# Optimization experiments

Measured on AMD Instinct MI355X. Metric: run time of the kernel, lower is better.

## Reference

```python
import jax, jax.numpy as jnp
import numpy as np

INV_TEMP = 10.0

def pairwise_distance(x, y):
    # squared L2 distance: [b,n,c],[b,m,c] -> [b,n,m]
    x2 = jnp.sum(x * x, axis=-1, keepdims=True)          # [b,n,1]
    y2 = jnp.sum(y * y, axis=-1)[:, None, :]             # [b,1,m]
    xy = jnp.einsum('bnc,bmc->bnm', x, y)                # [b,n,m]
    return x2 + y2 - 2.0 * xy

def setup_inputs() -> dict:
    key = jax.random.key(0)
    k1, k2, k3 = jax.random.split(key, 3)
    b, n, m, c = 4, 4096, 4096, 32
    x_f = jax.random.normal(k1, (b, n, c), dtype=jnp.float32)
    y_f = jax.random.normal(k2, (b, m, c), dtype=jnp.float32)
    y_c = jax.random.normal(k3, (b, m, 3), dtype=jnp.float32)
    temp_inv = jnp.ones((1,), dtype=jnp.float32) * INV_TEMP
    return {"x_f": x_f, "y_f": y_f, "y_c": y_c, "temp_inv": temp_inv}

def reference(x_f, y_f, y_c, temp_inv):
    # corr_type='soft', st=True (straight-through)
    dist = pairwise_distance(x_f, y_f)                   # [b,n,m]
    y_soft = jax.nn.softmax(-dist * temp_inv[0], axis=2) # [b,n,m]
    index = jnp.argmax(y_soft, axis=2)                   # [b,n]
    y_hard = jax.nn.one_hot(index, y_soft.shape[2], dtype=y_soft.dtype)
    ret = y_hard - jax.lax.stop_gradient(y_soft) + y_soft
    x_corr = jnp.matmul(ret, y_c)                        # [b,n,3]
    return x_corr
```

## Files before the change

### kernel.cpp

```cpp
#include <hip/hip_runtime.h>

#define B 4
#define N 4096
#define M 4096
#define C 32
#define BN (B * N)
#define MS 16

typedef short bf16x8 __attribute__((ext_vector_type(8)));
typedef float f32x4  __attribute__((ext_vector_type(4)));
typedef unsigned int u32x4 __attribute__((ext_vector_type(4)));

#define WS_WI ((size_t)MS * BN * 4)
#define WS_YP (WS_WI * 2)
#define WS_Y2 (WS_YP + (size_t)B * M * C * 3 * 2)

__device__ __forceinline__ float bf16lo(unsigned int u) { return __uint_as_float(u << 16); }
__device__ __forceinline__ float bf16hi(unsigned int u) { return __uint_as_float(u & 0xffff0000u); }

__device__ __forceinline__ void split3(const float f[8], bf16x8& h, bf16x8& m, bf16x8& l) {
    u32x4 hw, mw, lw;
    #pragma unroll
    for (int p = 0; p < 4; ++p) {
        const float f0 = f[2*p], f1 = f[2*p+1];
        const unsigned int h0 = __float_as_uint(f0) & 0xffff0000u;
        const unsigned int h1 = __float_as_uint(f1) & 0xffff0000u;
        hw[p] = h1 | (h0 >> 16);
        const float r0 = f0 - __uint_as_float(h0);
        const float r1 = f1 - __uint_as_float(h1);
        const unsigned int m0 = __float_as_uint(r0) & 0xffff0000u;
        const unsigned int m1 = __float_as_uint(r1) & 0xffff0000u;
        mw[p] = m1 | (m0 >> 16);
        const float s0 = r0 - __uint_as_float(m0);
        const float s1 = r1 - __uint_as_float(m1);
        lw[p] = (__float_as_uint(s1) & 0xffff0000u) | (__float_as_uint(s0) >> 16);
    }
    h = __builtin_bit_cast(bf16x8, hw);
    m = __builtin_bit_cast(bf16x8, mw);
    l = __builtin_bit_cast(bf16x8, lw);
}

__global__ __launch_bounds__(256)
void y_prepass(const void* __restrict__ yptr, const unsigned short* __restrict__ tptr,
               void* __restrict__ ws) {
    if (tptr[0] == 0x4120) return;
    unsigned short* yp = (unsigned short*)((char*)ws + WS_YP);
    float*          y2 = (float*)((char*)ws + WS_Y2);

    const int gid = blockIdx.x * 256 + threadIdx.x;
    const int row = gid >> 2;
    const int seg = gid & 3;
    const int b   = row >> 12;
    const int m   = row & 4095;
    const int chunk = m >> 8;
    const int mr    = m & 255;
    const float* p = (const float*)yptr + (size_t)row * C + seg * 8;
    float4 v0 = *(const float4*)p;
    float4 v1 = *(const float4*)(p + 4);
    const float f[8] = {v0.x, v0.y, v0.z, v0.w, v1.x, v1.y, v1.z, v1.w};

    bf16x8 h, m_, l;
    split3(f, h, m_, l);
    const size_t base = (size_t)((b * 16 + chunk) * 3) * 8192 + mr * 32 + seg * 8;
    *(bf16x8*)(yp + base)            = h;
    *(bf16x8*)(yp + base + 8192)     = m_;
    *(bf16x8*)(yp + base + 16384)    = l;

    float s = 0.f;
    #pragma unroll
    for (int k = 0; k < 8; ++k) s = fmaf(f[k], f[k], s);
    s += __shfl_xor(s, 1, 64);
    s += __shfl_xor(s, 2, 64);
    if (seg == 0) y2[row] = -0.5f * s;
}

__global__ __launch_bounds__(256, 3)
void nn_main(const void* __restrict__ xptr, const void* __restrict__ yptr,
             const unsigned short* __restrict__ tptr, void* __restrict__ ws) {
    float* wD = (float*)ws;
    int*   wI = (int*)((char*)ws + WS_WI);
    const bool is_bf16 = (tptr[0] == 0x4120);

    __shared__ uint4 bpl[3072];
    __shared__ float y2s[256];

    const int tid  = threadIdx.x;
    const int lane = tid & 63;
    const int wv   = tid >> 6;
    const int col  = lane & 15;
    const int quad = lane >> 4;
    const int bi   = blockIdx.x;
    const int ms   = bi & 15;
    const int nb   = (bi >> 4) & 15;
    const int b    = bi >> 8;
    const int n_base = nb * 256 + wv * 64;
    const int m0   = ms * 256;

    float bD[4][4];
    int   bI[4][4];
    #pragma unroll
    for (int t = 0; t < 4; ++t)
        #pragma unroll
        for (int r = 0; r < 4; ++r) { bD[t][r] = -__builtin_inff(); bI[t][r] = 0; }

    if (is_bf16) {
        const unsigned short* yp = (const unsigned short*)yptr;
        const unsigned short* xp = (const unsigned short*)xptr;

        {
            const int r = tid;
            const uint4* p = (const uint4*)(yp + ((size_t)b * M + m0 + r) * C);
            float s = 0.f;
            #pragma unroll
            for (int i = 0; i < 4; ++i) {
                uint4 v = p[i];
                float f;
                f = bf16lo(v.x); s = fmaf(f, f, s); f = bf16hi(v.x); s = fmaf(f, f, s);
                f = bf16lo(v.y); s = fmaf(f, f, s); f = bf16hi(v.y); s = fmaf(f, f, s);
                f = bf16lo(v.z); s = fmaf(f, f, s); f = bf16hi(v.z); s = fmaf(f, f, s);
                f = bf16lo(v.w); s = fmaf(f, f, s); f = bf16hi(v.w); s = fmaf(f, f, s);
            }
            y2s[r] = -0.5f * s;
        }

        bf16x8 af[4];
        #pragma unroll
        for (int t = 0; t < 4; ++t)
            af[t] = *(const bf16x8*)(xp + ((size_t)b * N + n_base + t * 16 + col) * C + quad * 8);

        __syncthreads();

        const unsigned short* yb = yp + ((size_t)b * M + m0) * C;
        const size_t boff = (size_t)col * C + quad * 8;
        bf16x8 bfr = *(const bf16x8*)(yb + boff);
        for (int mt = 0; mt < 16; ++mt) {
            bf16x8 bnx = bfr;
            if (mt < 15) bnx = *(const bf16x8*)(yb + boff + (size_t)(mt + 1) * (16 * C));
            const float y2c  = y2s[mt * 16 + col];
            const int   mcur = m0 + mt * 16 + col;
            #pragma unroll
            for (int t = 0; t < 4; ++t) {
                f32x4 acc = {y2c, y2c, y2c, y2c};
                acc = __builtin_amdgcn_mfma_f32_16x16x32_bf16(af[t], bfr, acc, 0, 0, 0);
                #pragma unroll
                for (int r = 0; r < 4; ++r)
                    if (acc[r] > bD[t][r]) { bD[t][r] = acc[r]; bI[t][r] = mcur; }
            }
            bfr = bnx;
        }
    } else {
        const uint4* src = (const uint4*)((char*)ws + WS_YP + (size_t)((b * 16 + ms) * 3) * 16384);
        const float* y2g = (const float*)((char*)ws + WS_Y2) + (size_t)b * M + m0;

        #pragma unroll
        for (int i = 0; i < 12; ++i) bpl[tid + i * 256] = src[tid + i * 256];
        y2s[tid] = y2g[tid];

        const float* xp = (const float*)xptr;
        bf16x8 ah[4], am[4], al[4];
        #pragma unroll
        for (int t = 0; t < 4; ++t) {
            const float* xr = xp + ((size_t)b * N + n_base + t * 16 + col) * C + quad * 8;
            float4 v0 = *(const float4*)xr;
            float4 v1 = *(const float4*)(xr + 4);
            const float xf[8] = {v0.x, v0.y, v0.z, v0.w, v1.x, v1.y, v1.z, v1.w};
            split3(xf, ah[t], am[t], al[t]);
        }

        __syncthreads();

        const unsigned short* lds = (const unsigned short*)bpl;
        const int fo = col * 32 + quad * 8;

        bf16x8 bh  = *(const bf16x8*)(lds + fo);
        bf16x8 bmi = *(const bf16x8*)(lds + 8192 + fo);
        bf16x8 bl  = *(const bf16x8*)(lds + 16384 + fo);
        for (int mt = 0; mt < 16; ++mt) {
            bf16x8 nh = bh, nm = bmi, nl = bl;
            if (mt < 15) {
                const int no = fo + (mt + 1) * (16 * 32);
                nh = *(const bf16x8*)(lds + no);
                nm = *(const bf16x8*)(lds + 8192 + no);
                nl = *(const bf16x8*)(lds + 16384 + no);
            }
            const float y2c  = y2s[mt * 16 + col];
            const int   mcur = m0 + mt * 16 + col;
            #pragma unroll
            for (int t = 0; t < 4; ++t) {
                f32x4 acc = {y2c, y2c, y2c, y2c};
                acc = __builtin_amdgcn_mfma_f32_16x16x32_bf16(am[t], bmi, acc, 0, 0, 0);
                acc = __builtin_amdgcn_mfma_f32_16x16x32_bf16(ah[t], bl,  acc, 0, 0, 0);
                acc = __builtin_amdgcn_mfma_f32_16x16x32_bf16(al[t], bh,  acc, 0, 0, 0);
                acc = __builtin_amdgcn_mfma_f32_16x16x32_bf16(ah[t], bmi, acc, 0, 0, 0);
                acc = __builtin_amdgcn_mfma_f32_16x16x32_bf16(am[t], bh,  acc, 0, 0, 0);
                acc = __builtin_amdgcn_mfma_f32_16x16x32_bf16(ah[t], bh,  acc, 0, 0, 0);
                #pragma unroll
                for (int r = 0; r < 4; ++r)
                    if (acc[r] > bD[t][r]) { bD[t][r] = acc[r]; bI[t][r] = mcur; }
            }
            bh = nh; bmi = nm; bl = nl;
        }
    }

    #pragma unroll
    for (int mask = 1; mask < 16; mask <<= 1) {
        #pragma unroll
        for (int t = 0; t < 4; ++t)
            #pragma unroll
            for (int r = 0; r < 4; ++r) {
                float oD = __shfl_xor(bD[t][r], mask, 64);
                int   oI = __shfl_xor(bI[t][r], mask, 64);
                if (oD > bD[t][r] || (oD == bD[t][r] && oI < bI[t][r])) {
                    bD[t][r] = oD; bI[t][r] = oI;
                }
            }
    }

    if (col == 0) {
        #pragma unroll
        for (int t = 0; t < 4; ++t)
            #pragma unroll
            for (int r = 0; r < 4; ++r) {
                const int n = n_base + t * 16 + quad * 4 + r;
                const size_t g = (size_t)ms * BN + (size_t)b * N + n;
                wD[g] = bD[t][r];
                wI[g] = bI[t][r];
            }
    }
}

__global__ __launch_bounds__(256)
void nn_combine(const float* __restrict__ wD, const int* __restrict__ wI,
                const void* __restrict__ ycptr,
                const unsigned short* __restrict__ tptr,
                void* __restrict__ outptr) {
    const bool is_bf16 = (tptr[0] == 0x4120);
    const int tid  = threadIdx.x;
    const int lane = tid & 63;
    const int wv   = tid >> 6;
    const int s    = lane >> 2;
    const int ro   = lane & 3;
    const int row  = blockIdx.x * 16 + wv * 4 + ro;

    float k  = wD[(size_t)s * BN + row];
    int   ix = wI[(size_t)s * BN + row];
    #pragma unroll
    for (int mask = 4; mask < 64; mask <<= 1) {
        float ok = __shfl_xor(k, mask, 64);
        int   oi = __shfl_xor(ix, mask, 64);
        if (ok > k || (ok == k && oi < ix)) { k = ok; ix = oi; }
    }

    if (s == 0) {
        const int b = row >> 12;
        const size_t src = ((size_t)b * M + ix) * 3;
        if (is_bf16) {
            const unsigned short* yc = (const unsigned short*)ycptr;
            unsigned short* o = (unsigned short*)outptr;
            o[row*3+0] = yc[src+0];
            o[row*3+1] = yc[src+1];
            o[row*3+2] = yc[src+2];
        } else {
            const float* yc = (const float*)ycptr;
            float* o = (float*)outptr;
            o[row*3+0] = yc[src+0];
            o[row*3+1] = yc[src+1];
            o[row*3+2] = yc[src+2];
        }
    }
}

extern "C" void kernel_launch(void* const* d_in, const int* in_sizes, int n_in,
                              void* d_out, int out_size, void* d_ws, size_t ws_size,
                              hipStream_t stream) {
    const void* x  = d_in[0];
    const void* y  = d_in[1];
    const void* yc = d_in[2];
    const unsigned short* t = (const unsigned short*)d_in[3];

    float* wD = (float*)d_ws;
    int*   wI = (int*)((char*)d_ws + WS_WI);

    y_prepass<<<256, 256, 0, stream>>>(y, t, d_ws);
    nn_main<<<1024, 256, 0, stream>>>(x, y, t, d_ws);
    nn_combine<<<1024, 256, 0, stream>>>(wD, wI, yc, t, d_out);
}
```

Measured before the change: 94.69 us.

## Stream low bf16 part of y from global, swizzle LDS, raise occupancy

The y low-order bf16 component is no longer staged through shared memory; it is stored row-major in the workspace and read directly from global/L2 in the inner loop. This cuts the LDS footprint from 48KB to 32KB per block, so launch bounds are raised to 4 blocks per CU. The high and mid components now use an XOR-swizzled layout to reduce LDS bank conflicts. The trade-off is extra global load latency on the critical path of each MFMA tile.

```diff
diff --git a/kernel.cpp b/kernel.cpp
--- a/kernel.cpp
+++ b/kernel.cpp
@@ -11,9 +11,10 @@
 typedef float f32x4  __attribute__((ext_vector_type(4)));
 typedef unsigned int u32x4 __attribute__((ext_vector_type(4)));
 
-#define WS_WI ((size_t)MS * BN * 4)
-#define WS_YP (WS_WI * 2)
-#define WS_Y2 (WS_YP + (size_t)B * M * C * 3 * 2)
+#define WS_WI  ((size_t)MS * BN * 4)
+#define WS_YHM (WS_WI * 2)
+#define WS_YL  (WS_YHM + (size_t)B * M * C * 2 * 2)
+#define WS_Y2  (WS_YL + (size_t)B * M * C * 2)
 
 __device__ __forceinline__ float bf16lo(unsigned int u) { return __uint_as_float(u << 16); }
 __device__ __forceinline__ float bf16hi(unsigned int u) { return __uint_as_float(u & 0xffff0000u); }
@@ -44,8 +45,9 @@
 void y_prepass(const void* __restrict__ yptr, const unsigned short* __restrict__ tptr,
                void* __restrict__ ws) {
     if (tptr[0] == 0x4120) return;
-    unsigned short* yp = (unsigned short*)((char*)ws + WS_YP);
-    float*          y2 = (float*)((char*)ws + WS_Y2);
+    unsigned short* yhm = (unsigned short*)((char*)ws + WS_YHM);
+    unsigned short* ylp = (unsigned short*)((char*)ws + WS_YL);
+    float*          y2  = (float*)((char*)ws + WS_Y2);
 
     const int gid = blockIdx.x * 256 + threadIdx.x;
     const int row = gid >> 2;
@@ -54,6 +56,9 @@
     const int m   = row & 4095;
     const int chunk = m >> 8;
     const int mr    = m & 255;
+    const int mt    = mr >> 4;
+    const int colr  = mr & 15;
+    const int segs  = seg ^ ((colr >> 1) & 3);
     const float* p = (const float*)yptr + (size_t)row * C + seg * 8;
     float4 v0 = *(const float4*)p;
     float4 v1 = *(const float4*)(p + 4);
@@ -61,10 +66,10 @@
 
     bf16x8 h, m_, l;
     split3(f, h, m_, l);
-    const size_t base = (size_t)((b * 16 + chunk) * 3) * 8192 + mr * 32 + seg * 8;
-    *(bf16x8*)(yp + base)            = h;
-    *(bf16x8*)(yp + base + 8192)     = m_;
-    *(bf16x8*)(yp + base + 16384)    = l;
+    const size_t hmbase = (size_t)(b * 16 + chunk) * 16384 + mt * 512 + colr * 32 + segs * 8;
+    *(bf16x8*)(yhm + hmbase)        = h;
+    *(bf16x8*)(yhm + hmbase + 8192) = m_;
+    *(bf16x8*)(ylp + (size_t)row * C + seg * 8) = l;
 
     float s = 0.f;
     #pragma unroll
@@ -74,14 +79,14 @@
     if (seg == 0) y2[row] = -0.5f * s;
 }
 
-__global__ __launch_bounds__(256, 3)
+__global__ __launch_bounds__(256, 4)
 void nn_main(const void* __restrict__ xptr, const void* __restrict__ yptr,
              const unsigned short* __restrict__ tptr, void* __restrict__ ws) {
     float* wD = (float*)ws;
     int*   wI = (int*)((char*)ws + WS_WI);
     const bool is_bf16 = (tptr[0] == 0x4120);
 
-    __shared__ uint4 bpl[3072];
+    __shared__ uint4 bpl[2048];
     __shared__ float y2s[256];
 
     const int tid  = threadIdx.x;
@@ -149,11 +154,12 @@
             bfr = bnx;
         }
     } else {
-        const uint4* src = (const uint4*)((char*)ws + WS_YP + (size_t)((b * 16 + ms) * 3) * 16384);
+        const uint4* src = (const uint4*)((char*)ws + WS_YHM + (size_t)(b * 16 + ms) * 32768);
         const float* y2g = (const float*)((char*)ws + WS_Y2) + (size_t)b * M + m0;
-
-        #pragma unroll
-        for (int i = 0; i < 12; ++i) bpl[tid + i * 256] = src[tid + i * 256];
+        const unsigned short* ylb = (const unsigned short*)((char*)ws + WS_YL) + ((size_t)b * M + m0) * C;
+
+        #pragma unroll
+        for (int i = 0; i < 8; ++i) bpl[tid + i * 256] = src[tid + i * 256];
         y2s[tid] = y2g[tid];
 
         const float* xp = (const float*)xptr;
@@ -170,18 +176,19 @@
         __syncthreads();
 
         const unsigned short* lds = (const unsigned short*)bpl;
-        const int fo = col * 32 + quad * 8;
+        const int fo   = col * 32 + (quad ^ ((col >> 1) & 3)) * 8;
+        const size_t lo = (size_t)col * C + quad * 8;
 
         bf16x8 bh  = *(const bf16x8*)(lds + fo);
         bf16x8 bmi = *(const bf16x8*)(lds + 8192 + fo);
-        bf16x8 bl  = *(const bf16x8*)(lds + 16384 + fo);
+        bf16x8 bl  = *(const bf16x8*)(ylb + lo);
         for (int mt = 0; mt < 16; ++mt) {
             bf16x8 nh = bh, nm = bmi, nl = bl;
             if (mt < 15) {
-                const int no = fo + (mt + 1) * (16 * 32);
+                const int no = fo + (mt + 1) * 512;
                 nh = *(const bf16x8*)(lds + no);
                 nm = *(const bf16x8*)(lds + 8192 + no);
-                nl = *(const bf16x8*)(lds + 16384 + no);
+                nl = *(const bf16x8*)(ylb + lo + (size_t)(mt + 1) * 512);
             }
             const float y2c  = y2s[mt * 16 + col];
             const int   mcur = m0 + mt * 16 + col;
```

Result: faster. 92.60 us (-2.2%).

## Fuse y split prepass into main kernel with smaller m-chunks and swizzled LDS

Applied to the files above, without the earlier changes.

Removes the separate y_prepass kernel. Each nn_main block now splits its own 128-row y chunk into three bf16 parts and computes the norms directly into swizzled LDS, rather than reading a precomputed global buffer. The m-split doubles from 16 to 32, giving 2048 blocks and halving LDS per block so occupancy can rise to 4 blocks per CU. The combine kernel reduces 32 partials per row. This saves a kernel launch and a global round trip, but the split arithmetic on y is now repeated by every n-block, and twice as many partial results are written and combined.

```diff
diff --git a/kernel.cpp b/kernel.cpp
--- a/kernel.cpp
+++ b/kernel.cpp
@@ -5,15 +5,13 @@
 #define M 4096
 #define C 32
 #define BN (B * N)
-#define MS 16
+#define MS 32
 
 typedef short bf16x8 __attribute__((ext_vector_type(8)));
 typedef float f32x4  __attribute__((ext_vector_type(4)));
 typedef unsigned int u32x4 __attribute__((ext_vector_type(4)));
 
 #define WS_WI ((size_t)MS * BN * 4)
-#define WS_YP (WS_WI * 2)
-#define WS_Y2 (WS_YP + (size_t)B * M * C * 3 * 2)
 
 __device__ __forceinline__ float bf16lo(unsigned int u) { return __uint_as_float(u << 16); }
 __device__ __forceinline__ float bf16hi(unsigned int u) { return __uint_as_float(u & 0xffff0000u); }
@@ -40,49 +38,15 @@
     l = __builtin_bit_cast(bf16x8, lw);
 }
 
-__global__ __launch_bounds__(256)
-void y_prepass(const void* __restrict__ yptr, const unsigned short* __restrict__ tptr,
-               void* __restrict__ ws) {
-    if (tptr[0] == 0x4120) return;
-    unsigned short* yp = (unsigned short*)((char*)ws + WS_YP);
-    float*          y2 = (float*)((char*)ws + WS_Y2);
-
-    const int gid = blockIdx.x * 256 + threadIdx.x;
-    const int row = gid >> 2;
-    const int seg = gid & 3;
-    const int b   = row >> 12;
-    const int m   = row & 4095;
-    const int chunk = m >> 8;
-    const int mr    = m & 255;
-    const float* p = (const float*)yptr + (size_t)row * C + seg * 8;
-    float4 v0 = *(const float4*)p;
-    float4 v1 = *(const float4*)(p + 4);
-    const float f[8] = {v0.x, v0.y, v0.z, v0.w, v1.x, v1.y, v1.z, v1.w};
-
-    bf16x8 h, m_, l;
-    split3(f, h, m_, l);
-    const size_t base = (size_t)((b * 16 + chunk) * 3) * 8192 + mr * 32 + seg * 8;
-    *(bf16x8*)(yp + base)            = h;
-    *(bf16x8*)(yp + base + 8192)     = m_;
-    *(bf16x8*)(yp + base + 16384)    = l;
-
-    float s = 0.f;
-    #pragma unroll
-    for (int k = 0; k < 8; ++k) s = fmaf(f[k], f[k], s);
-    s += __shfl_xor(s, 1, 64);
-    s += __shfl_xor(s, 2, 64);
-    if (seg == 0) y2[row] = -0.5f * s;
-}
-
-__global__ __launch_bounds__(256, 3)
+__global__ __launch_bounds__(256, 4)
 void nn_main(const void* __restrict__ xptr, const void* __restrict__ yptr,
              const unsigned short* __restrict__ tptr, void* __restrict__ ws) {
     float* wD = (float*)ws;
     int*   wI = (int*)((char*)ws + WS_WI);
     const bool is_bf16 = (tptr[0] == 0x4120);
 
-    __shared__ uint4 bpl[3072];
-    __shared__ float y2s[256];
+    __shared__ unsigned short ypl[12288];
+    __shared__ float y2s[128];
 
     const int tid  = threadIdx.x;
     const int lane = tid & 63;
@@ -90,11 +54,11 @@
     const int col  = lane & 15;
     const int quad = lane >> 4;
     const int bi   = blockIdx.x;
-    const int ms   = bi & 15;
-    const int nb   = (bi >> 4) & 15;
-    const int b    = bi >> 8;
+    const int ms   = bi & 31;
+    const int nb   = (bi >> 5) & 15;
+    const int b    = bi >> 9;
     const int n_base = nb * 256 + wv * 64;
-    const int m0   = ms * 256;
+    const int m0   = ms * 128;
 
     float bD[4][4];
     int   bI[4][4];
@@ -107,7 +71,7 @@
         const unsigned short* yp = (const unsigned short*)yptr;
         const unsigned short* xp = (const unsigned short*)xptr;
 
-        {
+        if (tid < 128) {
             const int r = tid;
             const uint4* p = (const uint4*)(yp + ((size_t)b * M + m0 + r) * C);
             float s = 0.f;
@@ -133,9 +97,9 @@
         const unsigned short* yb = yp + ((size_t)b * M + m0) * C;
         const size_t boff = (size_t)col * C + quad * 8;
         bf16x8 bfr = *(const bf16x8*)(yb + boff);
-        for (int mt = 0; mt < 16; ++mt) {
+        for (int mt = 0; mt < 8; ++mt) {
             bf16x8 bnx = bfr;
-            if (mt < 15) bnx = *(const bf16x8*)(yb + boff + (size_t)(mt + 1) * (16 * C));
+            if (mt < 7) bnx = *(const bf16x8*)(yb + boff + (size_t)(mt + 1) * (16 * C));
             const float y2c  = y2s[mt * 16 + col];
             const int   mcur = m0 + mt * 16 + col;
             #pragma unroll
@@ -149,14 +113,34 @@
             bfr = bnx;
         }
     } else {
-        const uint4* src = (const uint4*)((char*)ws + WS_YP + (size_t)((b * 16 + ms) * 3) * 16384);
-        const float* y2g = (const float*)((char*)ws + WS_Y2) + (size_t)b * M + m0;
-
-        #pragma unroll
-        for (int i = 0; i < 12; ++i) bpl[tid + i * 256] = src[tid + i * 256];
-        y2s[tid] = y2g[tid];
-
+        const float* yp = (const float*)yptr;
         const float* xp = (const float*)xptr;
+
+        #pragma unroll
+        for (int i = 0; i < 2; ++i) {
+            const int item = tid + i * 256;
+            const int r    = item >> 2;
+            const int seg  = item & 3;
+            const float* p = yp + ((size_t)b * M + m0 + r) * C + seg * 8;
+            float4 v0 = *(const float4*)p;
+            float4 v1 = *(const float4*)(p + 4);
+            const float f[8] = {v0.x, v0.y, v0.z, v0.w, v1.x, v1.y, v1.z, v1.w};
+
+            bf16x8 h, m_, l;
+            split3(f, h, m_, l);
+            const int base = ((r >> 4) << 9) + ((r & 15) << 5) + ((seg ^ ((r >> 1) & 3)) << 3);
+            *(bf16x8*)(ypl + base)        = h;
+            *(bf16x8*)(ypl + 4096 + base) = m_;
+            *(bf16x8*)(ypl + 8192 + base) = l;
+
+            float s = 0.f;
+            #pragma unroll
+            for (int k = 0; k < 8; ++k) s = fmaf(f[k], f[k], s);
+            s += __shfl_xor(s, 1, 64);
+            s += __shfl_xor(s, 2, 64);
+            if (seg == 0) y2s[r] = -0.5f * s;
+        }
+
         bf16x8 ah[4], am[4], al[4];
         #pragma unroll
         for (int t = 0; t < 4; ++t) {
@@ -169,19 +153,18 @@
 
         __syncthreads();
 
-        const unsigned short* lds = (const unsigned short*)bpl;
-        const int fo = col * 32 + quad * 8;
-
-        bf16x8 bh  = *(const bf16x8*)(lds + fo);
-        bf16x8 bmi = *(const bf16x8*)(lds + 8192 + fo);
-        bf16x8 bl  = *(const bf16x8*)(lds + 16384 + fo);
-        for (int mt = 0; mt < 16; ++mt) {
+        const int fo = col * 32 + (quad ^ ((col >> 1) & 3)) * 8;
+
+        bf16x8 bh  = *(const bf16x8*)(ypl + fo);
+        bf16x8 bmi = *(const bf16x8*)(ypl + 4096 + fo);
+        bf16x8 bl  = *(const bf16x8*)(ypl + 8192 + fo);
+        for (int mt = 0; mt < 8; ++mt) {
             bf16x8 nh = bh, nm = bmi, nl = bl;
-            if (mt < 15) {
-                const int no = fo + (mt + 1) * (16 * 32);
-                nh = *(const bf16x8*)(lds + no);
-                nm = *(const bf16x8*)(lds + 8192 + no);
-                nl = *(const bf16x8*)(lds + 16384 + no);
+            if (mt < 7) {
+                const int no = fo + (mt + 1) * 512;
+                nh = *(const bf16x8*)(ypl + no);
+                nm = *(const bf16x8*)(ypl + 4096 + no);
+                nl = *(const bf16x8*)(ypl + 8192 + no);
             }
             const float y2c  = y2s[mt * 16 + col];
             const int   mcur = m0 + mt * 16 + col;
@@ -238,14 +221,14 @@
     const int tid  = threadIdx.x;
     const int lane = tid & 63;
     const int wv   = tid >> 6;
-    const int s    = lane >> 2;
-    const int ro   = lane & 3;
-    const int row  = blockIdx.x * 16 + wv * 4 + ro;
+    const int s    = lane & 31;
+    const int half = lane >> 5;
+    const int row  = blockIdx.x * 8 + wv * 2 + half;
 
     float k  = wD[(size_t)s * BN + row];
     int   ix = wI[(size_t)s * BN + row];
     #pragma unroll
-    for (int mask = 4; mask < 64; mask <<= 1) {
+    for (int mask = 1; mask < 32; mask <<= 1) {
         float ok = __shfl_xor(k, mask, 64);
         int   oi = __shfl_xor(ix, mask, 64);
         if (ok > k || (ok == k && oi < ix)) { k = ok; ix = oi; }
@@ -281,7 +264,6 @@
     float* wD = (float*)d_ws;
     int*   wI = (int*)((char*)d_ws + WS_WI);
 
-    y_prepass<<<256, 256, 0, stream>>>(y, t, d_ws);
-    nn_main<<<1024, 256, 0, stream>>>(x, y, t, d_ws);
-    nn_combine<<<1024, 256, 0, stream>>>(wD, wI, yc, t, d_out);
-}
+    nn_main<<<2048, 256, 0, stream>>>(x, y, t, d_ws);
+    nn_combine<<<2048, 256, 0, stream>>>(wD, wI, yc, t, d_out);
+}
```

After: 101.2 us. 6.8% more time.
